# Kernel tuning notes

Measured on AMD Instinct MI355X. Metric: run time of the kernel, lower is better.

## Reference

```python
import jax, jax.numpy as jnp
import numpy as np

NUM_FEAT = 10

def _flatten(x):
    # [B,T,C,H,W] -> [B,C,T*H*W]
    B, T, C, H, W = x.shape
    return jnp.transpose(x, (0, 2, 1, 3, 4)).reshape(B, C, T * H * W)

def _conv1x1(w, b, x):
    # pointwise Conv1d: w [F,C], b [F], x [B,C,N] -> [B,F,N]
    return jnp.einsum('fc,bcn->bfn', w, x) + b[None, :, None]

def setup_inputs() -> dict:
    key = jax.random.key(0)
    ks = jax.random.split(key, 9)
    B, T, C, H, W = 1, 5, 64, 32, 32
    F = NUM_FEAT
    return {
        'input1': jax.random.normal(ks[0], (B, T, C, H, W), jnp.float32),
        'input2': jax.random.normal(ks[1], (B, T, C, H, W), jnp.float32),
        'act_weights': jax.random.uniform(ks[2], (3,), jnp.float32),
        'conv1_w': jax.random.normal(ks[3], (F, C), jnp.float32) * 0.05,
        'conv1_b': jnp.zeros((F,), jnp.float32),
        'conv2_w': jax.random.normal(ks[4], (F, C), jnp.float32) * 0.05,
        'conv2_b': jnp.zeros((F,), jnp.float32),
        'g3_w': jax.random.normal(ks[5], (F, C), jnp.float32) * 0.05,
        'g3_b': jnp.zeros((F,), jnp.float32),
    }

def reference(input1, input2, act_weights, conv1_w, conv1_b, conv2_w, conv2_b, g3_w, g3_b):
    B, T, C, H, W = input1.shape
    F = conv1_w.shape[0]
    x1 = _flatten(input1)                    # [B,C,N]
    x2 = _flatten(input2)                    # [B,C,N]
    q = _conv1x1(conv1_w, conv1_b, x1)       # [B,F,N]
    k = _conv1x1(conv2_w, conv2_b, x2)       # [B,F,N]
    v = _conv1x1(g3_w, g3_b, x1)             # [B,F,N]
    scores = jnp.einsum('bfn,bfm->bnm', q, k)  # [B,N,N] (same math, computed once)

    def branch(act_scores):
        o = jnp.einsum('bnm,bfm->bnf', act_scores, v)      # [B,N,F]
        o = o.reshape(B, T, H, W, F)
        return jnp.transpose(o, (0, 1, 4, 2, 3))           # [B,T,F,H,W]

    out = act_weights[0] * branch(jax.nn.relu(scores))
    out = out + act_weights[1] * branch(jax.nn.sigmoid(scores))
    # NOTE: original code scales the softmax branch by act_weights[0] (bug kept faithfully)
    out = out + act_weights[0] * branch(jax.nn.softmax(scores, axis=1))
    return out
```

## Files before the change

kernel.cpp:

```cpp
#include <hip/hip_runtime.h>

#define N_TOK   5120
#define C_IN    64
#define F_OUT   10
#define FP      12

#define DTILE   80
#define MTILE   40

__global__ __launch_bounds__(256) void qkv_kernel(
    const float* __restrict__ x1, const float* __restrict__ x2,
    const float* __restrict__ w1, const float* __restrict__ b1,
    const float* __restrict__ w2, const float* __restrict__ b2,
    const float* __restrict__ w3, const float* __restrict__ b3,
    float* __restrict__ Q, float* __restrict__ K, float* __restrict__ V)
{
    __shared__ float sw[3][C_IN][F_OUT];
    __shared__ float psum[3][4][64][11];
    int tid = threadIdx.x;
    for (int i = tid; i < C_IN * F_OUT; i += 256) {
        int f = i >> 6, c = i & 63;
        sw[0][c][f] = w1[i];
        sw[1][c][f] = w2[i];
        sw[2][c][f] = w3[i];
    }
    __syncthreads();

    int g = tid >> 6, l = tid & 63;
    int n = blockIdx.x * 64 + l;
    int t = n >> 10, p = n & 1023;
    const float* x1p = x1 + t * (C_IN * 1024) + p;
    const float* x2p = x2 + t * (C_IN * 1024) + p;

    float qa[F_OUT], ka[F_OUT], va[F_OUT];
#pragma unroll
    for (int f = 0; f < F_OUT; ++f) { qa[f] = 0.f; ka[f] = 0.f; va[f] = 0.f; }

    int c0 = g * 16;
#pragma unroll 4
    for (int cc = 0; cc < 16; ++cc) {
        int c = c0 + cc;
        float a = x1p[c * 1024];
        float b = x2p[c * 1024];
#pragma unroll
        for (int f = 0; f < F_OUT; ++f) {
            qa[f] = fmaf(sw[0][c][f], a, qa[f]);
            ka[f] = fmaf(sw[1][c][f], b, ka[f]);
            va[f] = fmaf(sw[2][c][f], a, va[f]);
        }
    }
#pragma unroll
    for (int f = 0; f < F_OUT; ++f) {
        psum[0][g][l][f] = qa[f];
        psum[1][g][l][f] = ka[f];
        psum[2][g][l][f] = va[f];
    }
    __syncthreads();

    for (int i = tid; i < 3 * 64 * F_OUT; i += 256) {
        int a = i / 640;
        int rem = i - a * 640;
        int nl = rem / 10, f = rem - nl * 10;
        float s = psum[a][0][nl][f] + psum[a][1][nl][f] +
                  psum[a][2][nl][f] + psum[a][3][nl][f];
        const float* bias = (a == 0) ? b1 : (a == 1) ? b2 : b3;
        float* dst = (a == 0) ? Q : (a == 1) ? K : V;
        dst[(blockIdx.x * 64 + nl) * FP + f] = s + bias[f];
    }
    for (int i = tid; i < 3 * 64 * 2; i += 256) {
        int a = i / 128;
        int rem = i - a * 128;
        int nl = rem >> 1, pd = rem & 1;
        float* dst = (a == 0) ? Q : (a == 1) ? K : V;
        dst[(blockIdx.x * 64 + nl) * FP + 10 + pd] = 0.f;
    }
}

__global__ __launch_bounds__(256) void denom_kernel(
    const float* __restrict__ Q, const float* __restrict__ K,
    float* __restrict__ dpart, int nclen)
{
    int mTile = blockIdx.x % 10;
    int nc    = blockIdx.x / 10;
    int tid   = threadIdx.x;
    int m0 = mTile * 512 + tid;
    int m1 = m0 + 256;

    float k0[12], k1[12];
    {
        const float4* kp = (const float4*)(K + m0 * FP);
        float4 a = kp[0], b = kp[1], c = kp[2];
        k0[0]=a.x; k0[1]=a.y; k0[2]=a.z; k0[3]=a.w;
        k0[4]=b.x; k0[5]=b.y; k0[6]=b.z; k0[7]=b.w;
        k0[8]=c.x; k0[9]=c.y; k0[10]=c.z; k0[11]=c.w;
    }
    {
        const float4* kp = (const float4*)(K + m1 * FP);
        float4 a = kp[0], b = kp[1], c = kp[2];
        k1[0]=a.x; k1[1]=a.y; k1[2]=a.z; k1[3]=a.w;
        k1[4]=b.x; k1[5]=b.y; k1[6]=b.z; k1[7]=b.w;
        k1[8]=c.x; k1[9]=c.y; k1[10]=c.z; k1[11]=c.w;
    }

    __shared__ __align__(16) float sq[DTILE * FP];

    float d0 = 0.f, d1 = 0.f;
    int n0 = nc * nclen;
    for (int base = n0; base < n0 + nclen; base += DTILE) {
        __syncthreads();
        if (tid < DTILE * FP / 4)
            ((float4*)sq)[tid] = ((const float4*)(Q + base * FP))[tid];
        __syncthreads();
#pragma unroll 4
        for (int j = 0; j < DTILE; ++j) {
            const float4* qp = (const float4*)(sq + j * FP);
            float4 qa = qp[0], qb = qp[1], qc = qp[2];
            float qq[12] = {qa.x, qa.y, qa.z, qa.w, qb.x, qb.y, qb.z, qb.w,
                            qc.x, qc.y, qc.z, qc.w};
            float s0 = 0.f, s1 = 0.f;
#pragma unroll
            for (int f = 0; f < F_OUT; ++f) {
                s0 = fmaf(qq[f], k0[f], s0);
                s1 = fmaf(qq[f], k1[f], s1);
            }
            d0 += __expf(fminf(s0, 60.f));
            d1 += __expf(fminf(s1, 60.f));
        }
    }
    dpart[nc * N_TOK + m0] = d0;
    dpart[nc * N_TOK + m1] = d1;
}

__global__ __launch_bounds__(256) void invw_kernel(
    const float* __restrict__ dpart, const float* __restrict__ aw,
    float* __restrict__ invw, int nchunks)
{
    int m = blockIdx.x * 256 + threadIdx.x;
    float d = 0.f;
#pragma unroll 8
    for (int c = 0; c < nchunks; ++c) d += dpart[c * N_TOK + m];
    invw[m] = aw[0] / d;
}

__global__ __launch_bounds__(256) void main_kernel(
    const float* __restrict__ Q, const float* __restrict__ K,
    const float* __restrict__ V, const float* __restrict__ invw,
    const float* __restrict__ aw, float* __restrict__ opart, int mclen)
{
    int nTile = blockIdx.x % 5;
    int mc    = blockIdx.x / 5;
    int tid   = threadIdx.x;
    int nb = nTile * 1024 + tid;
    float w0 = aw[0], w1v = aw[1];

    float q[4][12];
#pragma unroll
    for (int r = 0; r < 4; ++r) {
        const float4* qp = (const float4*)(Q + (nb + r * 256) * FP);
        float4 a = qp[0], b = qp[1], c = qp[2];
        q[r][0]=a.x; q[r][1]=a.y; q[r][2]=a.z; q[r][3]=a.w;
        q[r][4]=b.x; q[r][5]=b.y; q[r][6]=b.z; q[r][7]=b.w;
        q[r][8]=c.x; q[r][9]=c.y; q[r][10]=c.z; q[r][11]=c.w;
    }

    float acc[4][F_OUT];
#pragma unroll
    for (int r = 0; r < 4; ++r)
#pragma unroll
        for (int f = 0; f < F_OUT; ++f) acc[r][f] = 0.f;

    __shared__ __align__(16) float sk[MTILE * FP];
    __shared__ __align__(16) float sv[MTILE * FP];
    __shared__ __align__(16) float siw[MTILE];

    int mstart = mc * mclen;
    for (int mbase = mstart; mbase < mstart + mclen; mbase += MTILE) {
        __syncthreads();
        if (tid < 120)
            ((float4*)sk)[tid] = ((const float4*)(K + mbase * FP))[tid];
        else if (tid < 240)
            ((float4*)sv)[tid - 120] = ((const float4*)(V + mbase * FP))[tid - 120];
        else if (tid < 250)
            ((float4*)siw)[tid - 240] = ((const float4*)(invw + mbase))[tid - 240];
        __syncthreads();

#pragma unroll 2
        for (int j = 0; j < MTILE; ++j) {
            const float4* kp = (const float4*)(sk + j * FP);
            float4 ka = kp[0], kb = kp[1], kc = kp[2];
            float kk[12] = {ka.x, ka.y, ka.z, ka.w, kb.x, kb.y, kb.z, kb.w,
                            kc.x, kc.y, kc.z, kc.w};
            const float4* vp = (const float4*)(sv + j * FP);
            float4 va = vp[0], vb = vp[1], vc = vp[2];
            float vv[12] = {va.x, va.y, va.z, va.w, vb.x, vb.y, vb.z, vb.w,
                            vc.x, vc.y, vc.z, vc.w};
            float iw = siw[j];

#pragma unroll
            for (int r = 0; r < 4; ++r) {
                float s = 0.f;
#pragma unroll
                for (int f = 0; f < F_OUT; ++f) s = fmaf(q[r][f], kk[f], s);
                float rl = fmaxf(s, 0.f);
                float e  = __expf(fminf(s, 60.f));
                float sg = e * __builtin_amdgcn_rcpf(1.f + e);
                float cf = fmaf(e, iw, fmaf(w1v, sg, w0 * rl));
#pragma unroll
                for (int f = 0; f < F_OUT; ++f) acc[r][f] = fmaf(cf, vv[f], acc[r][f]);
            }
        }
    }

#pragma unroll
    for (int r = 0; r < 4; ++r) {
        float2* o = (float2*)(opart + (size_t)(mc * N_TOK + nb + r * 256) * F_OUT);
#pragma unroll
        for (int f = 0; f < 5; ++f)
            o[f] = make_float2(acc[r][2 * f], acc[r][2 * f + 1]);
    }
}

__global__ __launch_bounds__(256) void reduce_kernel(
    const float* __restrict__ opart, float* __restrict__ out, int mchunks)
{
    int idx = blockIdx.x * 256 + threadIdx.x;
    float s = 0.f;
#pragma unroll 8
    for (int c = 0; c < mchunks; ++c) s += opart[c * (N_TOK * F_OUT) + idx];
    unsigned un = (unsigned)idx / 10u;
    int n = (int)un;
    int f = idx - n * 10;
    int t = n >> 10, p = n & 1023;
    out[((t * F_OUT + f) << 10) + p] = s;
}

extern "C" void kernel_launch(void* const* d_in, const int* in_sizes, int n_in,
                              void* d_out, int out_size, void* d_ws, size_t ws_size,
                              hipStream_t stream)
{
    const float* in1 = (const float*)d_in[0];
    const float* in2 = (const float*)d_in[1];
    const float* aw  = (const float*)d_in[2];
    const float* w1  = (const float*)d_in[3];
    const float* b1  = (const float*)d_in[4];
    const float* w2  = (const float*)d_in[5];
    const float* b2  = (const float*)d_in[6];
    const float* w3  = (const float*)d_in[7];
    const float* b3  = (const float*)d_in[8];
    float* out = (float*)d_out;

    int nchunks, mchunks;
    if (ws_size >= (size_t)30 << 20)      { nchunks = 64; mchunks = 128; }
    else if (ws_size >= (size_t)16 << 20) { nchunks = 64; mchunks = 64;  }
    else                                  { nchunks = 16; mchunks = 32;  }
    int nclen = N_TOK / nchunks;
    int mclen = N_TOK / mchunks;

    float* ws    = (float*)d_ws;
    float* Q     = ws;
    float* K     = Q + N_TOK * FP;
    float* V     = K + N_TOK * FP;
    float* invw  = V + N_TOK * FP;
    float* dpart = invw + N_TOK;
    float* opart = dpart + nchunks * N_TOK;

    qkv_kernel<<<N_TOK / 64, 256, 0, stream>>>(in1, in2, w1, b1, w2, b2, w3, b3, Q, K, V);
    denom_kernel<<<10 * nchunks, 256, 0, stream>>>(Q, K, dpart, nclen);
    invw_kernel<<<N_TOK / 256, 256, 0, stream>>>(dpart, aw, invw, nchunks);
    main_kernel<<<5 * mchunks, 256, 0, stream>>>(Q, K, V, invw, aw, opart, mclen);
    reduce_kernel<<<(N_TOK * F_OUT) / 256, 256, 0, stream>>>(opart, out, mchunks);
}
```

Before: 137.7 us.

## Retile attention kernels, pack inverse denominators into K padding, simplify QKV projection

The QKV projection now uses one thread per output element over 600 blocks, with weights held in registers, replacing the shared-memory partial-sum reduction. The denominator kernel processes four key rows per thread, and the main kernel processes five query rows per thread over four n-tiles. The per-key inverse softmax weight is stored in K's unused padding column, so the separate invw tile load is no longer needed. Chunk counts and unroll factors were retuned. These changes trade higher register pressure and fewer blocks for more reuse per shared-memory load, with some risk of lower occupancy.

After: 137.0 us. No clear change (-0.5%).

```diff
diff --git a/kernel.cpp b/kernel.cpp
--- a/kernel.cpp
+++ b/kernel.cpp
@@ -5,7 +5,7 @@
 #define F_OUT   10
 #define FP      12
 
-#define DTILE   80
+#define DTILE   40
 #define MTILE   40
 
 __global__ __launch_bounds__(256) void qkv_kernel(
@@ -15,163 +15,127 @@
     const float* __restrict__ w3, const float* __restrict__ b3,
     float* __restrict__ Q, float* __restrict__ K, float* __restrict__ V)
 {
-    __shared__ float sw[3][C_IN][F_OUT];
-    __shared__ float psum[3][4][64][11];
-    int tid = threadIdx.x;
-    for (int i = tid; i < C_IN * F_OUT; i += 256) {
-        int f = i >> 6, c = i & 63;
-        sw[0][c][f] = w1[i];
-        sw[1][c][f] = w2[i];
-        sw[2][c][f] = w3[i];
-    }
-    __syncthreads();
-
-    int g = tid >> 6, l = tid & 63;
-    int n = blockIdx.x * 64 + l;
+    int arr = blockIdx.x / 200;
+    int rem = blockIdx.x - arr * 200;
+    int f   = rem / 20;
+    int nbk = rem - f * 20;
+    int n   = nbk * 256 + threadIdx.x;
     int t = n >> 10, p = n & 1023;
-    const float* x1p = x1 + t * (C_IN * 1024) + p;
-    const float* x2p = x2 + t * (C_IN * 1024) + p;
-
-    float qa[F_OUT], ka[F_OUT], va[F_OUT];
-#pragma unroll
-    for (int f = 0; f < F_OUT; ++f) { qa[f] = 0.f; ka[f] = 0.f; va[f] = 0.f; }
-
-    int c0 = g * 16;
-#pragma unroll 4
-    for (int cc = 0; cc < 16; ++cc) {
-        int c = c0 + cc;
-        float a = x1p[c * 1024];
-        float b = x2p[c * 1024];
-#pragma unroll
-        for (int f = 0; f < F_OUT; ++f) {
-            qa[f] = fmaf(sw[0][c][f], a, qa[f]);
-            ka[f] = fmaf(sw[1][c][f], b, ka[f]);
-            va[f] = fmaf(sw[2][c][f], a, va[f]);
-        }
-    }
-#pragma unroll
-    for (int f = 0; f < F_OUT; ++f) {
-        psum[0][g][l][f] = qa[f];
-        psum[1][g][l][f] = ka[f];
-        psum[2][g][l][f] = va[f];
-    }
-    __syncthreads();
-
-    for (int i = tid; i < 3 * 64 * F_OUT; i += 256) {
-        int a = i / 640;
-        int rem = i - a * 640;
-        int nl = rem / 10, f = rem - nl * 10;
-        float s = psum[a][0][nl][f] + psum[a][1][nl][f] +
-                  psum[a][2][nl][f] + psum[a][3][nl][f];
-        const float* bias = (a == 0) ? b1 : (a == 1) ? b2 : b3;
-        float* dst = (a == 0) ? Q : (a == 1) ? K : V;
-        dst[(blockIdx.x * 64 + nl) * FP + f] = s + bias[f];
-    }
-    for (int i = tid; i < 3 * 64 * 2; i += 256) {
-        int a = i / 128;
-        int rem = i - a * 128;
-        int nl = rem >> 1, pd = rem & 1;
-        float* dst = (a == 0) ? Q : (a == 1) ? K : V;
-        dst[(blockIdx.x * 64 + nl) * FP + 10 + pd] = 0.f;
-    }
+
+    const float* x    = (arr == 1) ? x2 : x1;
+    const float* w    = (arr == 0) ? w1 : (arr == 1) ? w2 : w3;
+    const float* bias = (arr == 0) ? b1 : (arr == 1) ? b2 : b3;
+    float*       dst  = (arr == 0) ? Q  : (arr == 1) ? K  : V;
+
+    const float* xp = x + t * (C_IN * 1024) + p;
+    const float* wr = w + f * C_IN;
+
+    float4 wv[16];
+#pragma unroll
+    for (int i = 0; i < 16; ++i) wv[i] = ((const float4*)wr)[i];
+
+    float acc = 0.f;
+#pragma unroll
+    for (int i = 0; i < 16; ++i) {
+        acc = fmaf(wv[i].x, xp[(4 * i + 0) * 1024], acc);
+        acc = fmaf(wv[i].y, xp[(4 * i + 1) * 1024], acc);
+        acc = fmaf(wv[i].z, xp[(4 * i + 2) * 1024], acc);
+        acc = fmaf(wv[i].w, xp[(4 * i + 3) * 1024], acc);
+    }
+    dst[n * FP + f] = acc + bias[f];
 }
 
 __global__ __launch_bounds__(256) void denom_kernel(
     const float* __restrict__ Q, const float* __restrict__ K,
     float* __restrict__ dpart, int nclen)
 {
-    int mTile = blockIdx.x % 10;
-    int nc    = blockIdx.x / 10;
+    int mTile = blockIdx.x % 5;
+    int nc    = blockIdx.x / 5;
     int tid   = threadIdx.x;
-    int m0 = mTile * 512 + tid;
-    int m1 = m0 + 256;
-
-    float k0[12], k1[12];
-    {
-        const float4* kp = (const float4*)(K + m0 * FP);
-        float4 a = kp[0], b = kp[1], c = kp[2];
-        k0[0]=a.x; k0[1]=a.y; k0[2]=a.z; k0[3]=a.w;
-        k0[4]=b.x; k0[5]=b.y; k0[6]=b.z; k0[7]=b.w;
-        k0[8]=c.x; k0[9]=c.y; k0[10]=c.z; k0[11]=c.w;
-    }
-    {
-        const float4* kp = (const float4*)(K + m1 * FP);
-        float4 a = kp[0], b = kp[1], c = kp[2];
-        k1[0]=a.x; k1[1]=a.y; k1[2]=a.z; k1[3]=a.w;
-        k1[4]=b.x; k1[5]=b.y; k1[6]=b.z; k1[7]=b.w;
-        k1[8]=c.x; k1[9]=c.y; k1[10]=c.z; k1[11]=c.w;
+    int m0 = mTile * 1024 + tid;
+
+    float kk[4][10];
+#pragma unroll
+    for (int c = 0; c < 4; ++c) {
+        const float* kp = K + (m0 + c * 256) * FP;
+        float4 a = ((const float4*)kp)[0];
+        float4 b = ((const float4*)kp)[1];
+        float2 e = ((const float2*)kp)[4];
+        kk[c][0]=a.x; kk[c][1]=a.y; kk[c][2]=a.z; kk[c][3]=a.w;
+        kk[c][4]=b.x; kk[c][5]=b.y; kk[c][6]=b.z; kk[c][7]=b.w;
+        kk[c][8]=e.x; kk[c][9]=e.y;
     }
 
     __shared__ __align__(16) float sq[DTILE * FP];
 
-    float d0 = 0.f, d1 = 0.f;
+    float d[4] = {0.f, 0.f, 0.f, 0.f};
     int n0 = nc * nclen;
     for (int base = n0; base < n0 + nclen; base += DTILE) {
         __syncthreads();
         if (tid < DTILE * FP / 4)
             ((float4*)sq)[tid] = ((const float4*)(Q + base * FP))[tid];
         __syncthreads();
-#pragma unroll 4
+#pragma unroll 2
         for (int j = 0; j < DTILE; ++j) {
             const float4* qp = (const float4*)(sq + j * FP);
             float4 qa = qp[0], qb = qp[1], qc = qp[2];
-            float qq[12] = {qa.x, qa.y, qa.z, qa.w, qb.x, qb.y, qb.z, qb.w,
-                            qc.x, qc.y, qc.z, qc.w};
-            float s0 = 0.f, s1 = 0.f;
-#pragma unroll
-            for (int f = 0; f < F_OUT; ++f) {
-                s0 = fmaf(qq[f], k0[f], s0);
-                s1 = fmaf(qq[f], k1[f], s1);
+            float qq[10] = {qa.x, qa.y, qa.z, qa.w, qb.x, qb.y, qb.z, qb.w,
+                            qc.x, qc.y};
+#pragma unroll
+            for (int c = 0; c < 4; ++c) {
+                float s = 0.f;
+#pragma unroll
+                for (int f = 0; f < F_OUT; ++f) s = fmaf(qq[f], kk[c][f], s);
+                d[c] += __expf(fminf(s, 60.f));
             }
-            d0 += __expf(fminf(s0, 60.f));
-            d1 += __expf(fminf(s1, 60.f));
         }
     }
-    dpart[nc * N_TOK + m0] = d0;
-    dpart[nc * N_TOK + m1] = d1;
+#pragma unroll
+    for (int c = 0; c < 4; ++c) dpart[nc * N_TOK + m0 + c * 256] = d[c];
 }
 
 __global__ __launch_bounds__(256) void invw_kernel(
     const float* __restrict__ dpart, const float* __restrict__ aw,
-    float* __restrict__ invw, int nchunks)
+    float* __restrict__ K, int nchunks)
 {
     int m = blockIdx.x * 256 + threadIdx.x;
     float d = 0.f;
 #pragma unroll 8
     for (int c = 0; c < nchunks; ++c) d += dpart[c * N_TOK + m];
-    invw[m] = aw[0] / d;
+    K[m * FP + 10] = aw[0] / d;
 }
 
 __global__ __launch_bounds__(256) void main_kernel(
     const float* __restrict__ Q, const float* __restrict__ K,
-    const float* __restrict__ V, const float* __restrict__ invw,
-    const float* __restrict__ aw, float* __restrict__ opart, int mclen)
-{
-    int nTile = blockIdx.x % 5;
-    int mc    = blockIdx.x / 5;
+    const float* __restrict__ V, const float* __restrict__ aw,
+    float* __restrict__ opart, int mclen)
+{
+    int nTile = blockIdx.x % 4;
+    int mc    = blockIdx.x / 4;
     int tid   = threadIdx.x;
-    int nb = nTile * 1024 + tid;
+    int nb = nTile * 1280 + tid;
     float w0 = aw[0], w1v = aw[1];
 
-    float q[4][12];
-#pragma unroll
-    for (int r = 0; r < 4; ++r) {
-        const float4* qp = (const float4*)(Q + (nb + r * 256) * FP);
-        float4 a = qp[0], b = qp[1], c = qp[2];
+    float q[5][10];
+#pragma unroll
+    for (int r = 0; r < 5; ++r) {
+        const float* qp = Q + (nb + r * 256) * FP;
+        float4 a = ((const float4*)qp)[0];
+        float4 b = ((const float4*)qp)[1];
+        float2 e = ((const float2*)qp)[4];
         q[r][0]=a.x; q[r][1]=a.y; q[r][2]=a.z; q[r][3]=a.w;
         q[r][4]=b.x; q[r][5]=b.y; q[r][6]=b.z; q[r][7]=b.w;
-        q[r][8]=c.x; q[r][9]=c.y; q[r][10]=c.z; q[r][11]=c.w;
-    }
-
-    float acc[4][F_OUT];
-#pragma unroll
-    for (int r = 0; r < 4; ++r)
+        q[r][8]=e.x; q[r][9]=e.y;
+    }
+
+    float acc[5][F_OUT];
+#pragma unroll
+    for (int r = 0; r < 5; ++r)
 #pragma unroll
         for (int f = 0; f < F_OUT; ++f) acc[r][f] = 0.f;
 
     __shared__ __align__(16) float sk[MTILE * FP];
     __shared__ __align__(16) float sv[MTILE * FP];
-    __shared__ __align__(16) float siw[MTILE];
 
     int mstart = mc * mclen;
     for (int mbase = mstart; mbase < mstart + mclen; mbase += MTILE) {
@@ -180,24 +144,22 @@
             ((float4*)sk)[tid] = ((const float4*)(K + mbase * FP))[tid];
         else if (tid < 240)
             ((float4*)sv)[tid - 120] = ((const float4*)(V + mbase * FP))[tid - 120];
-        else if (tid < 250)
-            ((float4*)siw)[tid - 240] = ((const float4*)(invw + mbase))[tid - 240];
         __syncthreads();
 
 #pragma unroll 2
         for (int j = 0; j < MTILE; ++j) {
             const float4* kp = (const float4*)(sk + j * FP);
             float4 ka = kp[0], kb = kp[1], kc = kp[2];
-            float kk[12] = {ka.x, ka.y, ka.z, ka.w, kb.x, kb.y, kb.z, kb.w,
-                            kc.x, kc.y, kc.z, kc.w};
+            float kk[10] = {ka.x, ka.y, ka.z, ka.w, kb.x, kb.y, kb.z, kb.w,
+                            kc.x, kc.y};
+            float iw = kc.z;
             const float4* vp = (const float4*)(sv + j * FP);
             float4 va = vp[0], vb = vp[1], vc = vp[2];
-            float vv[12] = {va.x, va.y, va.z, va.w, vb.x, vb.y, vb.z, vb.w,
-                            vc.x, vc.y, vc.z, vc.w};
-            float iw = siw[j];
-
-#pragma unroll
-            for (int r = 0; r < 4; ++r) {
+            float vv[10] = {va.x, va.y, va.z, va.w, vb.x, vb.y, vb.z, vb.w,
+                            vc.x, vc.y};
+
+#pragma unroll
+            for (int r = 0; r < 5; ++r) {
                 float s = 0.f;
 #pragma unroll
                 for (int f = 0; f < F_OUT; ++f) s = fmaf(q[r][f], kk[f], s);
@@ -212,7 +174,7 @@
     }
 
 #pragma unroll
-    for (int r = 0; r < 4; ++r) {
+    for (int r = 0; r < 5; ++r) {
         float2* o = (float2*)(opart + (size_t)(mc * N_TOK + nb + r * 256) * F_OUT);
 #pragma unroll
         for (int f = 0; f < 5; ++f)
@@ -225,7 +187,7 @@
 {
     int idx = blockIdx.x * 256 + threadIdx.x;
     float s = 0.f;
-#pragma unroll 8
+#pragma unroll 16
     for (int c = 0; c < mchunks; ++c) s += opart[c * (N_TOK * F_OUT) + idx];
     unsigned un = (unsigned)idx / 10u;
     int n = (int)un;
@@ -250,9 +212,8 @@
     float* out = (float*)d_out;
 
     int nchunks, mchunks;
-    if (ws_size >= (size_t)30 << 20)      { nchunks = 64; mchunks = 128; }
-    else if (ws_size >= (size_t)16 << 20) { nchunks = 64; mchunks = 64;  }
-    else                                  { nchunks = 16; mchunks = 32;  }
+    if (ws_size >= (size_t)32 << 20) { nchunks = 128; mchunks = 128; }
+    else                             { nchunks = 32;  mchunks = 32;  }
     int nclen = N_TOK / nchunks;
     int mclen = N_TOK / mchunks;
 
@@ -260,13 +221,12 @@
     float* Q     = ws;
     float* K     = Q + N_TOK * FP;
     float* V     = K + N_TOK * FP;
-    float* invw  = V + N_TOK * FP;
-    float* dpart = invw + N_TOK;
+    float* dpart = V + N_TOK * FP;
     float* opart = dpart + nchunks * N_TOK;
 
-    qkv_kernel<<<N_TOK / 64, 256, 0, stream>>>(in1, in2, w1, b1, w2, b2, w3, b3, Q, K, V);
-    denom_kernel<<<10 * nchunks, 256, 0, stream>>>(Q, K, dpart, nclen);
-    invw_kernel<<<N_TOK / 256, 256, 0, stream>>>(dpart, aw, invw, nchunks);
-    main_kernel<<<5 * mchunks, 256, 0, stream>>>(Q, K, V, invw, aw, opart, mclen);
+    qkv_kernel<<<600, 256, 0, stream>>>(in1, in2, w1, b1, w2, b2, w3, b3, Q, K, V);
+    denom_kernel<<<5 * nchunks, 256, 0, stream>>>(Q, K, dpart, nclen);
+    invw_kernel<<<N_TOK / 256, 256, 0, stream>>>(dpart, aw, K, nchunks);
+    main_kernel<<<4 * mchunks, 256, 0, stream>>>(Q, K, V, aw, opart, mclen);
     reduce_kernel<<<(N_TOK * F_OUT) / 256, 256, 0, stream>>>(opart, out, mchunks);
 }
```
